# Kernel optimization log

Measured on AMD Instinct MI355X. Metric: run time of the kernel, lower is better.

## Reference

```python
import jax, jax.numpy as jnp
import numpy as np

N, F, FH, H = 4096, 512, 64, 8  # nodes, in-features, per-head out-features, heads
ALPHA = 0.2  # LeakyReLU slope


def setup_inputs() -> dict:
    key = jax.random.key(0)
    ks = jax.random.split(key, 6)
    X = jax.random.normal(ks[0], (N, F), dtype=jnp.float32)
    A = (jax.random.uniform(ks[1], (N, N)) < 0.02).astype(jnp.float32)
    glorot_w = (2.0 / (F + FH)) ** 0.5
    glorot_a = (2.0 / (FH + 1)) ** 0.5
    W = jax.random.normal(ks[2], (H, F, FH), dtype=jnp.float32) * glorot_w
    a_self = jax.random.normal(ks[3], (H, FH), dtype=jnp.float32) * glorot_a
    a_neigh = jax.random.normal(ks[4], (H, FH), dtype=jnp.float32) * glorot_a
    b = jnp.zeros((H, FH), dtype=jnp.float32)
    return {"X": X, "A": A, "W": W, "a_self": a_self, "a_neigh": a_neigh, "b": b}


def reference(X, A, W, a_self, a_neigh, b):
    # per-head linear projection: [H, N, FH]
    feats = jnp.einsum('nf,hfo->hno', X, W)
    s_self = jnp.einsum('hno,ho->hn', feats, a_self)    # [H, N]
    s_neigh = jnp.einsum('hno,ho->hn', feats, a_neigh)  # [H, N]
    # additive logits: self_i + neigh_j -> [H, N, N]
    dense = s_self[:, :, None] + s_neigh[:, None, :]
    dense = jnp.where(dense > 0, dense, ALPHA * dense)  # LeakyReLU(0.2)
    dense = dense * A[None, :, :]                       # multiplicative adjacency (as in source)
    attn = jax.nn.softmax(dense, axis=-1)               # full-row softmax (as in source)
    # dropout is identity at inference
    out = jnp.einsum('hij,hjo->hio', attn, feats) + b[:, None, :]  # [H, N, FH]
    out = jnp.transpose(out, (1, 0, 2)).reshape(N, H * FH)         # concat heads
    return jax.nn.relu(out)
```

## Files before the change

kernel.cpp:

```cpp
#include <hip/hip_runtime.h>
#include <hip/hip_bf16.h>

#define N_NODES 4096
#define F_IN 512
#define FHD 64
#define H_HEADS 8
#define C_OUT 512
#define ALPHA 0.2f
#define MAXE 192

typedef __attribute__((ext_vector_type(8))) short bf16x8;
typedef __attribute__((ext_vector_type(4))) float f32x4;

static __device__ __forceinline__ unsigned short f2bf(float f) {
  __hip_bfloat16 h = __float2bfloat16(f);
  union { __hip_bfloat16 h; unsigned short u; } cvt;
  cvt.h = h;
  return cvt.u;
}
static __device__ __forceinline__ float bf2f(unsigned short u) {
  return __uint_as_float(((unsigned)u) << 16);
}

__global__ __launch_bounds__(256) void conv_kernel(
    const float* __restrict__ X, const float* __restrict__ W,
    unsigned short* __restrict__ Xb, unsigned short* __restrict__ WbT,
    float* __restrict__ colsum) {
  __shared__ float sT[64][65];
  const int bid = blockIdx.x;
  const int tid = threadIdx.x;
  if (bid < 2048) {
    int idx = bid * 256 + tid;
    float4 v = reinterpret_cast<const float4*>(X)[idx];
    ushort4 u;
    u.x = f2bf(v.x); u.y = f2bf(v.y); u.z = f2bf(v.z); u.w = f2bf(v.w);
    reinterpret_cast<ushort4*>(Xb)[idx] = u;
  } else if (bid < 2048 + 64) {
    const int b2 = bid - 2048;
    const int fblk = b2 & 7, h = b2 >> 3;
#pragma unroll
    for (int i = 0; i < 16; ++i) {
      int idx = tid + i * 256;
      int f = idx >> 6, o = idx & 63;
      sT[f][o] = W[((size_t)h * F_IN + fblk * 64 + f) * FHD + o];
    }
    __syncthreads();
#pragma unroll
    for (int i = 0; i < 16; ++i) {
      int idx = tid + i * 256;
      int o = idx >> 6, f = idx & 63;
      WbT[(size_t)h * FHD * F_IN + (size_t)o * F_IN + fblk * 64 + f] =
          f2bf(sT[f][o]);
    }
  } else {
    colsum[tid] = 0.f;
    colsum[tid + 256] = 0.f;
  }
}

__global__ __launch_bounds__(256) void gemm_feats_mfma_kernel(
    const unsigned short* __restrict__ Xb, const unsigned short* __restrict__ WbT,
    const float* __restrict__ a_self, const float* __restrict__ a_neigh,
    unsigned short* __restrict__ featsb,
    float* __restrict__ s_self, float* __restrict__ s_neigh,
    float* __restrict__ colsum) {
  const int h = blockIdx.y;
  const int n0 = blockIdx.x * 64;
  __shared__ unsigned short sX[2][64 * 72];
  __shared__ unsigned short sW[2][64 * 72];
  __shared__ float sred[4][64];
  const int tid = threadIdx.x;
  const int wid = tid >> 6, lane = tid & 63;
  const int l15 = lane & 15, l4 = lane >> 4;

  const int row = tid >> 2, seg = (tid & 3) * 16;
  const unsigned short* xsrc = Xb + (size_t)(n0 + row) * F_IN + seg;
  const unsigned short* wsrc = WbT + ((size_t)h * FHD + row) * F_IN + seg;
  const int soff = row * 72 + seg;

  f32x4 acc[4];
#pragma unroll
  for (int j = 0; j < 4; ++j) acc[j] = (f32x4){0.f, 0.f, 0.f, 0.f};

  *(bf16x8*)&sX[0][soff] = *(const bf16x8*)(xsrc);
  *(bf16x8*)&sX[0][soff + 8] = *(const bf16x8*)(xsrc + 8);
  *(bf16x8*)&sW[0][soff] = *(const bf16x8*)(wsrc);
  *(bf16x8*)&sW[0][soff + 8] = *(const bf16x8*)(wsrc + 8);
  __syncthreads();

  int cur = 0;
  for (int s = 0; s < 8; ++s) {
    bf16x8 px0, px1, pw0, pw1;
    const bool pf = (s < 7);
    if (pf) {
      const int k = (s + 1) * 64;
      px0 = *(const bf16x8*)(xsrc + k);
      px1 = *(const bf16x8*)(xsrc + k + 8);
      pw0 = *(const bf16x8*)(wsrc + k);
      pw1 = *(const bf16x8*)(wsrc + k + 8);
    }
#pragma unroll
    for (int kk = 0; kk < 2; ++kk) {
      bf16x8 a = *(const bf16x8*)&sX[cur][(wid * 16 + l15) * 72 + kk * 32 + l4 * 8];
#pragma unroll
      for (int tn = 0; tn < 4; ++tn) {
        bf16x8 b = *(const bf16x8*)&sW[cur][(tn * 16 + l15) * 72 + kk * 32 + l4 * 8];
        acc[tn] =
            __builtin_amdgcn_mfma_f32_16x16x32_bf16(a, b, acc[tn], 0, 0, 0);
      }
    }
    if (pf) {
      *(bf16x8*)&sX[cur ^ 1][soff] = px0;
      *(bf16x8*)&sX[cur ^ 1][soff + 8] = px1;
      *(bf16x8*)&sW[cur ^ 1][soff] = pw0;
      *(bf16x8*)&sW[cur ^ 1][soff + 8] = pw1;
      __syncthreads();
      cur ^= 1;
    }
  }

  float aS[4], aN[4];
#pragma unroll
  for (int tn = 0; tn < 4; ++tn) {
    aS[tn] = a_self[h * FHD + tn * 16 + l15];
    aN[tn] = a_neigh[h * FHD + tn * 16 + l15];
  }
#pragma unroll
  for (int r = 0; r < 4; ++r) {
    const int grow = n0 + wid * 16 + l4 * 4 + r;
#pragma unroll
    for (int tn = 0; tn < 4; ++tn)
      featsb[(size_t)grow * C_OUT + h * FHD + tn * 16 + l15] =
          f2bf(acc[tn][r]);
    float ps = 0.f, pn = 0.f;
#pragma unroll
    for (int tn = 0; tn < 4; ++tn) {
      float v = acc[tn][r];
      ps = fmaf(v, aS[tn], ps);
      pn = fmaf(v, aN[tn], pn);
    }
#pragma unroll
    for (int sh = 1; sh < 16; sh <<= 1) {
      ps += __shfl_xor(ps, sh, 64);
      pn += __shfl_xor(pn, sh, 64);
    }
    if (l15 == 0) {
      s_self[grow * 8 + h] = ps;
      s_neigh[grow * 8 + h] = pn;
    }
  }

  float psum[4];
#pragma unroll
  for (int tn = 0; tn < 4; ++tn) {
    float s = acc[tn][0] + acc[tn][1] + acc[tn][2] + acc[tn][3];
    s += __shfl_xor(s, 16, 64);
    s += __shfl_xor(s, 32, 64);
    psum[tn] = s;
  }
  if (l4 == 0) {
#pragma unroll
    for (int tn = 0; tn < 4; ++tn) sred[wid][tn * 16 + l15] = psum[tn];
  }
  __syncthreads();
  if (tid < 64) {
    float s = sred[0][tid] + sred[1][tid] + sred[2][tid] + sred[3][tid];
    atomicAdd(&colsum[h * FHD + tid], s);
  }
}

__global__ __launch_bounds__(256) void attn_kernel(
    const float* __restrict__ A, const unsigned short* __restrict__ featsb,
    const float* __restrict__ s_self, const float* __restrict__ s_neigh,
    const float* __restrict__ colsum, const float* __restrict__ bias,
    float* __restrict__ out) {
  const int i = blockIdx.x;
  const int tid = threadIdx.x;
  const int wid = tid >> 6, lane = tid & 63;
  __shared__ int s_idx[MAXE];
  __shared__ float s_w[MAXE][9];
  __shared__ int wave_tot[4];
  __shared__ float sh_self[8];
  __shared__ float sh_e0[8], sh_invZ[8];

  if (tid < 8) sh_self[tid] = s_self[i * 8 + tid];

  const float4* __restrict__ Arow4 =
      reinterpret_cast<const float4*>(A + (size_t)i * N_NODES);
  float4 v[4];
#pragma unroll
  for (int q = 0; q < 4; ++q) v[q] = Arow4[tid * 4 + q];
  int mask16 = 0;
#pragma unroll
  for (int q = 0; q < 4; ++q) {
    mask16 |= (v[q].x != 0.f) ? (1 << (q * 4 + 0)) : 0;
    mask16 |= (v[q].y != 0.f) ? (1 << (q * 4 + 1)) : 0;
    mask16 |= (v[q].z != 0.f) ? (1 << (q * 4 + 2)) : 0;
    mask16 |= (v[q].w != 0.f) ? (1 << (q * 4 + 3)) : 0;
  }
  int cnt = __popc(mask16);
  int inc = cnt;
#pragma unroll
  for (int s = 1; s < 64; s <<= 1) {
    int t = __shfl_up(inc, s, 64);
    if (lane >= s) inc += t;
  }
  if (lane == 63) wave_tot[wid] = inc;
  __syncthreads();
  int wprefix = 0, tot = 0;
#pragma unroll
  for (int w = 0; w < 4; ++w) {
    int t = wave_tot[w];
    if (w < wid) wprefix += t;
    tot += t;
  }
  int pos = wprefix + inc - cnt;
  const int jbase = tid * 16;
  while (mask16) {
    int k = __ffs(mask16) - 1;
    mask16 &= mask16 - 1;
    if (pos < MAXE) s_idx[pos] = jbase + k;
    ++pos;
  }
  const int deg = tot < MAXE ? tot : MAXE;
  __syncthreads();

  for (int k = tid; k < deg * 8; k += 256) {
    int e = k >> 3, h = k & 7;
    int j = s_idx[e];
    float l = sh_self[h] + s_neigh[j * 8 + h];
    s_w[e][h] = l > 0.f ? l : ALPHA * l;
  }
  __syncthreads();

#pragma unroll
  for (int p = 0; p < 2; ++p) {
    const int h = wid * 2 + p;
    float m = -1e30f;
    for (int e = lane; e < deg; e += 64) m = fmaxf(m, s_w[e][h]);
#pragma unroll
    for (int s = 32; s > 0; s >>= 1) m = fmaxf(m, __shfl_xor(m, s, 64));
    m = fmaxf(m, 0.0f);
    float e0 = __expf(-m);
    float zs = 0.f;
    for (int e = lane; e < deg; e += 64) {
      float w = __expf(s_w[e][h] - m);
      s_w[e][h] = w - e0;
      zs += w;
    }
#pragma unroll
    for (int s = 32; s > 0; s >>= 1) zs += __shfl_xor(zs, s, 64);
    if (lane == 0) {
      sh_e0[h] = e0;
      sh_invZ[h] = 1.0f / (zs + (float)(N_NODES - deg) * e0);
    }
  }
  __syncthreads();

  const int h = tid >> 5;
  const float e0 = sh_e0[h], invZ = sh_invZ[h];
  const float2 cs = *reinterpret_cast<const float2*>(&colsum[tid * 2]);
  const ushort2* __restrict__ fb = reinterpret_cast<const ushort2*>(featsb);
  float ax0 = e0 * cs.x, ay0 = e0 * cs.y;
  float ax1 = 0.f, ay1 = 0.f, ax2 = 0.f, ay2 = 0.f, ax3 = 0.f, ay3 = 0.f;
  int e = 0;
  for (; e + 3 < deg; e += 4) {
    int j0 = s_idx[e], j1 = s_idx[e + 1], j2 = s_idx[e + 2], j3 = s_idx[e + 3];
    float w0 = s_w[e][h], w1 = s_w[e + 1][h];
    float w2 = s_w[e + 2][h], w3 = s_w[e + 3][h];
    ushort2 u0 = fb[(size_t)j0 * 256 + tid];
    ushort2 u1 = fb[(size_t)j1 * 256 + tid];
    ushort2 u2 = fb[(size_t)j2 * 256 + tid];
    ushort2 u3 = fb[(size_t)j3 * 256 + tid];
    ax0 = fmaf(w0, bf2f(u0.x), ax0);
    ay0 = fmaf(w0, bf2f(u0.y), ay0);
    ax1 = fmaf(w1, bf2f(u1.x), ax1);
    ay1 = fmaf(w1, bf2f(u1.y), ay1);
    ax2 = fmaf(w2, bf2f(u2.x), ax2);
    ay2 = fmaf(w2, bf2f(u2.y), ay2);
    ax3 = fmaf(w3, bf2f(u3.x), ax3);
    ay3 = fmaf(w3, bf2f(u3.y), ay3);
  }
  for (; e < deg; ++e) {
    float w0 = s_w[e][h];
    ushort2 u0 = fb[(size_t)s_idx[e] * 256 + tid];
    ax0 = fmaf(w0, bf2f(u0.x), ax0);
    ay0 = fmaf(w0, bf2f(u0.y), ay0);
  }
  const float2 bb = *reinterpret_cast<const float2*>(&bias[tid * 2]);
  float vx = ((ax0 + ax1) + (ax2 + ax3)) * invZ + bb.x;
  float vy = ((ay0 + ay1) + (ay2 + ay3)) * invZ + bb.y;
  float2 o;
  o.x = vx > 0.f ? vx : 0.f;
  o.y = vy > 0.f ? vy : 0.f;
  *reinterpret_cast<float2*>(&out[(size_t)i * C_OUT + tid * 2]) = o;
}

extern "C" void kernel_launch(void* const* d_in, const int* in_sizes, int n_in,
                              void* d_out, int out_size, void* d_ws, size_t ws_size,
                              hipStream_t stream) {
  const float* X = (const float*)d_in[0];
  const float* A = (const float*)d_in[1];
  const float* W = (const float*)d_in[2];
  const float* a_self = (const float*)d_in[3];
  const float* a_neigh = (const float*)d_in[4];
  const float* b = (const float*)d_in[5];
  float* out = (float*)d_out;

  char* ws = (char*)d_ws;
  unsigned short* featsb = (unsigned short*)ws;
  char* p = ws + (size_t)N_NODES * C_OUT * 2;
  float* s_self = (float*)p;  p += N_NODES * H_HEADS * 4;
  float* s_neigh = (float*)p; p += N_NODES * H_HEADS * 4;
  float* colsum = (float*)p;  p += C_OUT * 4;
  unsigned short* WbT = (unsigned short*)p;

  unsigned short* Xb = (unsigned short*)d_out;

  conv_kernel<<<2048 + 64 + 1, 256, 0, stream>>>(X, W, Xb, WbT, colsum);
  gemm_feats_mfma_kernel<<<dim3(64, 8), 256, 0, stream>>>(
      Xb, WbT, a_self, a_neigh, featsb, s_self, s_neigh, colsum);
  attn_kernel<<<N_NODES, 256, 0, stream>>>(A, featsb, s_self, s_neigh, colsum,
                                           b, out);
}
```

Before: 60.51 us.

## Move adjacency row scan into GEMM launch to overlap with projection

```diff
diff --git a/kernel.cpp b/kernel.cpp
--- a/kernel.cpp
+++ b/kernel.cpp
@@ -8,6 +8,7 @@
 #define C_OUT 512
 #define ALPHA 0.2f
 #define MAXE 192
+#define GEMM_BLOCKS 512
 
 typedef __attribute__((ext_vector_type(8))) short bf16x8;
 typedef __attribute__((ext_vector_type(4))) float f32x4;
@@ -58,19 +59,68 @@
   }
 }
 
-__global__ __launch_bounds__(256) void gemm_feats_mfma_kernel(
+__global__ __launch_bounds__(256) void gemm_scan_kernel(
     const unsigned short* __restrict__ Xb, const unsigned short* __restrict__ WbT,
     const float* __restrict__ a_self, const float* __restrict__ a_neigh,
+    const float* __restrict__ A,
     unsigned short* __restrict__ featsb,
     float* __restrict__ s_self, float* __restrict__ s_neigh,
-    float* __restrict__ colsum) {
-  const int h = blockIdx.y;
-  const int n0 = blockIdx.x * 64;
+    float* __restrict__ colsum,
+    unsigned short* __restrict__ edges, int* __restrict__ degs) {
   __shared__ unsigned short sX[2][64 * 72];
   __shared__ unsigned short sW[2][64 * 72];
   __shared__ float sred[4][64];
+  const int bid = blockIdx.x;
   const int tid = threadIdx.x;
   const int wid = tid >> 6, lane = tid & 63;
+
+  if (bid >= GEMM_BLOCKS) {
+    const int i = bid - GEMM_BLOCKS;
+    int* wave_tot = reinterpret_cast<int*>(&sred[0][0]);
+    const float4* __restrict__ Arow4 =
+        reinterpret_cast<const float4*>(A + (size_t)i * N_NODES);
+    float4 v[4];
+#pragma unroll
+    for (int q = 0; q < 4; ++q) v[q] = Arow4[tid * 4 + q];
+    int mask16 = 0;
+#pragma unroll
+    for (int q = 0; q < 4; ++q) {
+      mask16 |= (v[q].x != 0.f) ? (1 << (q * 4 + 0)) : 0;
+      mask16 |= (v[q].y != 0.f) ? (1 << (q * 4 + 1)) : 0;
+      mask16 |= (v[q].z != 0.f) ? (1 << (q * 4 + 2)) : 0;
+      mask16 |= (v[q].w != 0.f) ? (1 << (q * 4 + 3)) : 0;
+    }
+    int cnt = __popc(mask16);
+    int inc = cnt;
+#pragma unroll
+    for (int s = 1; s < 64; s <<= 1) {
+      int t = __shfl_up(inc, s, 64);
+      if (lane >= s) inc += t;
+    }
+    if (lane == 63) wave_tot[wid] = inc;
+    __syncthreads();
+    int wprefix = 0, tot = 0;
+#pragma unroll
+    for (int w = 0; w < 4; ++w) {
+      int t = wave_tot[w];
+      if (w < wid) wprefix += t;
+      tot += t;
+    }
+    int pos = wprefix + inc - cnt;
+    const int jbase = tid * 16;
+    unsigned short* __restrict__ erow = edges + (size_t)i * MAXE;
+    while (mask16) {
+      int k = __ffs(mask16) - 1;
+      mask16 &= mask16 - 1;
+      if (pos < MAXE) erow[pos] = (unsigned short)(jbase + k);
+      ++pos;
+    }
+    if (tid == 0) degs[i] = tot < MAXE ? tot : MAXE;
+    return;
+  }
+
+  const int h = bid >> 6;
+  const int n0 = (bid & 63) * 64;
   const int l15 = lane & 15, l4 = lane >> 4;
 
   const int row = tid >> 2, seg = (tid & 3) * 16;
@@ -158,6 +208,7 @@
     s += __shfl_xor(s, 32, 64);
     psum[tn] = s;
   }
+  __syncthreads();
   if (l4 == 0) {
 #pragma unroll
     for (int tn = 0; tn < 4; ++tn) sred[wid][tn * 16 + l15] = psum[tn];
@@ -170,7 +221,8 @@
 }
 
 __global__ __launch_bounds__(256) void attn_kernel(
-    const float* __restrict__ A, const unsigned short* __restrict__ featsb,
+    const unsigned short* __restrict__ edges, const int* __restrict__ degs,
+    const unsigned short* __restrict__ featsb,
     const float* __restrict__ s_self, const float* __restrict__ s_neigh,
     const float* __restrict__ colsum, const float* __restrict__ bias,
     float* __restrict__ out) {
@@ -179,50 +231,12 @@
   const int wid = tid >> 6, lane = tid & 63;
   __shared__ int s_idx[MAXE];
   __shared__ float s_w[MAXE][9];
-  __shared__ int wave_tot[4];
   __shared__ float sh_self[8];
   __shared__ float sh_e0[8], sh_invZ[8];
 
+  const int deg = degs[i];
   if (tid < 8) sh_self[tid] = s_self[i * 8 + tid];
-
-  const float4* __restrict__ Arow4 =
-      reinterpret_cast<const float4*>(A + (size_t)i * N_NODES);
-  float4 v[4];
-#pragma unroll
-  for (int q = 0; q < 4; ++q) v[q] = Arow4[tid * 4 + q];
-  int mask16 = 0;
-#pragma unroll
-  for (int q = 0; q < 4; ++q) {
-    mask16 |= (v[q].x != 0.f) ? (1 << (q * 4 + 0)) : 0;
-    mask16 |= (v[q].y != 0.f) ? (1 << (q * 4 + 1)) : 0;
-    mask16 |= (v[q].z != 0.f) ? (1 << (q * 4 + 2)) : 0;
-    mask16 |= (v[q].w != 0.f) ? (1 << (q * 4 + 3)) : 0;
-  }
-  int cnt = __popc(mask16);
-  int inc = cnt;
-#pragma unroll
-  for (int s = 1; s < 64; s <<= 1) {
-    int t = __shfl_up(inc, s, 64);
-    if (lane >= s) inc += t;
-  }
-  if (lane == 63) wave_tot[wid] = inc;
-  __syncthreads();
-  int wprefix = 0, tot = 0;
-#pragma unroll
-  for (int w = 0; w < 4; ++w) {
-    int t = wave_tot[w];
-    if (w < wid) wprefix += t;
-    tot += t;
-  }
-  int pos = wprefix + inc - cnt;
-  const int jbase = tid * 16;
-  while (mask16) {
-    int k = __ffs(mask16) - 1;
-    mask16 &= mask16 - 1;
-    if (pos < MAXE) s_idx[pos] = jbase + k;
-    ++pos;
-  }
-  const int deg = tot < MAXE ? tot : MAXE;
+  if (tid < deg) s_idx[tid] = edges[(size_t)i * MAXE + tid];
   __syncthreads();
 
   for (int k = tid; k < deg * 8; k += 256) {
@@ -313,13 +327,17 @@
   float* s_self = (float*)p;  p += N_NODES * H_HEADS * 4;
   float* s_neigh = (float*)p; p += N_NODES * H_HEADS * 4;
   float* colsum = (float*)p;  p += C_OUT * 4;
+  int* degs = (int*)p;        p += N_NODES * 4;
+  unsigned short* edges = (unsigned short*)p;
+  p += (size_t)N_NODES * MAXE * 2;
   unsigned short* WbT = (unsigned short*)p;
 
   unsigned short* Xb = (unsigned short*)d_out;
 
   conv_kernel<<<2048 + 64 + 1, 256, 0, stream>>>(X, W, Xb, WbT, colsum);
-  gemm_feats_mfma_kernel<<<dim3(64, 8), 256, 0, stream>>>(
-      Xb, WbT, a_self, a_neigh, featsb, s_self, s_neigh, colsum);
-  attn_kernel<<<N_NODES, 256, 0, stream>>>(A, featsb, s_self, s_neigh, colsum,
-                                           b, out);
-}
+  gemm_scan_kernel<<<GEMM_BLOCKS + N_NODES, 256, 0, stream>>>(
+      Xb, WbT, a_self, a_neigh, A, featsb, s_self, s_neigh, colsum, edges,
+      degs);
+  attn_kernel<<<N_NODES, 256, 0, stream>>>(edges, degs, featsb, s_self,
+                                           s_neigh, colsum, b, out);
+}
```

Measured after the change: 55.76 us. 7.9% less time.

## Move adjacency scan into first kernel and split attention gather across 512 threads

Applied to the files above, without the earlier changes.

```diff
diff --git a/kernel.cpp b/kernel.cpp
--- a/kernel.cpp
+++ b/kernel.cpp
@@ -22,21 +22,66 @@
   return __uint_as_float(((unsigned)u) << 16);
 }
 
-__global__ __launch_bounds__(256) void conv_kernel(
-    const float* __restrict__ X, const float* __restrict__ W,
-    unsigned short* __restrict__ Xb, unsigned short* __restrict__ WbT,
-    float* __restrict__ colsum) {
+__global__ __launch_bounds__(256) void stream_kernel(
+    const float* __restrict__ A, const float* __restrict__ X,
+    const float* __restrict__ W, unsigned short* __restrict__ edges,
+    int* __restrict__ degs, unsigned short* __restrict__ Xb,
+    unsigned short* __restrict__ WbT, float* __restrict__ colsum) {
+  __shared__ int wave_tot[4];
   __shared__ float sT[64][65];
   const int bid = blockIdx.x;
   const int tid = threadIdx.x;
-  if (bid < 2048) {
-    int idx = bid * 256 + tid;
+
+  if (bid < N_NODES) {
+    const int i = bid;
+    const int wid = tid >> 6, lane = tid & 63;
+    const float4* __restrict__ Arow4 =
+        reinterpret_cast<const float4*>(A + (size_t)i * N_NODES);
+    float4 v[4];
+#pragma unroll
+    for (int q = 0; q < 4; ++q) v[q] = Arow4[tid * 4 + q];
+    int mask16 = 0;
+#pragma unroll
+    for (int q = 0; q < 4; ++q) {
+      mask16 |= (v[q].x != 0.f) ? (1 << (q * 4 + 0)) : 0;
+      mask16 |= (v[q].y != 0.f) ? (1 << (q * 4 + 1)) : 0;
+      mask16 |= (v[q].z != 0.f) ? (1 << (q * 4 + 2)) : 0;
+      mask16 |= (v[q].w != 0.f) ? (1 << (q * 4 + 3)) : 0;
+    }
+    int cnt = __popc(mask16);
+    int inc = cnt;
+#pragma unroll
+    for (int s = 1; s < 64; s <<= 1) {
+      int t = __shfl_up(inc, s, 64);
+      if (lane >= s) inc += t;
+    }
+    if (lane == 63) wave_tot[wid] = inc;
+    __syncthreads();
+    int wprefix = 0, tot = 0;
+#pragma unroll
+    for (int w = 0; w < 4; ++w) {
+      int t = wave_tot[w];
+      if (w < wid) wprefix += t;
+      tot += t;
+    }
+    int pos = wprefix + inc - cnt;
+    const int jbase = tid * 16;
+    unsigned short* __restrict__ erow = edges + (size_t)i * MAXE;
+    while (mask16) {
+      int k = __ffs(mask16) - 1;
+      mask16 &= mask16 - 1;
+      if (pos < MAXE) erow[pos] = (unsigned short)(jbase + k);
+      ++pos;
+    }
+    if (tid == 0) degs[i] = tot < MAXE ? tot : MAXE;
+  } else if (bid < N_NODES + 2048) {
+    int idx = (bid - N_NODES) * 256 + tid;
     float4 v = reinterpret_cast<const float4*>(X)[idx];
     ushort4 u;
     u.x = f2bf(v.x); u.y = f2bf(v.y); u.z = f2bf(v.z); u.w = f2bf(v.w);
     reinterpret_cast<ushort4*>(Xb)[idx] = u;
-  } else if (bid < 2048 + 64) {
-    const int b2 = bid - 2048;
+  } else if (bid < N_NODES + 2048 + 64) {
+    const int b2 = bid - (N_NODES + 2048);
     const int fblk = b2 & 7, h = b2 >> 3;
 #pragma unroll
     for (int i = 0; i < 16; ++i) {
@@ -169,8 +214,9 @@
   }
 }
 
-__global__ __launch_bounds__(256) void attn_kernel(
-    const float* __restrict__ A, const unsigned short* __restrict__ featsb,
+__global__ __launch_bounds__(512) void attn_kernel(
+    const unsigned short* __restrict__ edges, const int* __restrict__ degs,
+    const unsigned short* __restrict__ featsb,
     const float* __restrict__ s_self, const float* __restrict__ s_neigh,
     const float* __restrict__ colsum, const float* __restrict__ bias,
     float* __restrict__ out) {
@@ -179,53 +225,16 @@
   const int wid = tid >> 6, lane = tid & 63;
   __shared__ int s_idx[MAXE];
   __shared__ float s_w[MAXE][9];
-  __shared__ int wave_tot[4];
   __shared__ float sh_self[8];
   __shared__ float sh_e0[8], sh_invZ[8];
-
+  __shared__ float s_part[256][2];
+
+  const int deg = degs[i];
   if (tid < 8) sh_self[tid] = s_self[i * 8 + tid];
-
-  const float4* __restrict__ Arow4 =
-      reinterpret_cast<const float4*>(A + (size_t)i * N_NODES);
-  float4 v[4];
-#pragma unroll
-  for (int q = 0; q < 4; ++q) v[q] = Arow4[tid * 4 + q];
-  int mask16 = 0;
-#pragma unroll
-  for (int q = 0; q < 4; ++q) {
-    mask16 |= (v[q].x != 0.f) ? (1 << (q * 4 + 0)) : 0;
-    mask16 |= (v[q].y != 0.f) ? (1 << (q * 4 + 1)) : 0;
-    mask16 |= (v[q].z != 0.f) ? (1 << (q * 4 + 2)) : 0;
-    mask16 |= (v[q].w != 0.f) ? (1 << (q * 4 + 3)) : 0;
-  }
-  int cnt = __popc(mask16);
-  int inc = cnt;
-#pragma unroll
-  for (int s = 1; s < 64; s <<= 1) {
-    int t = __shfl_up(inc, s, 64);
-    if (lane >= s) inc += t;
-  }
-  if (lane == 63) wave_tot[wid] = inc;
-  __syncthreads();
-  int wprefix = 0, tot = 0;
-#pragma unroll
-  for (int w = 0; w < 4; ++w) {
-    int t = wave_tot[w];
-    if (w < wid) wprefix += t;
-    tot += t;
-  }
-  int pos = wprefix + inc - cnt;
-  const int jbase = tid * 16;
-  while (mask16) {
-    int k = __ffs(mask16) - 1;
-    mask16 &= mask16 - 1;
-    if (pos < MAXE) s_idx[pos] = jbase + k;
-    ++pos;
-  }
-  const int deg = tot < MAXE ? tot : MAXE;
-  __syncthreads();
-
-  for (int k = tid; k < deg * 8; k += 256) {
+  if (tid < deg) s_idx[tid] = edges[(size_t)i * MAXE + tid];
+  __syncthreads();
+
+  for (int k = tid; k < deg * 8; k += 512) {
     int e = k >> 3, h = k & 7;
     int j = s_idx[e];
     float l = sh_self[h] + s_neigh[j * 8 + h];
@@ -233,9 +242,8 @@
   }
   __syncthreads();
 
-#pragma unroll
-  for (int p = 0; p < 2; ++p) {
-    const int h = wid * 2 + p;
+  {
+    const int h = wid;
     float m = -1e30f;
     for (int e = lane; e < deg; e += 64) m = fmaxf(m, s_w[e][h]);
 #pragma unroll
@@ -257,21 +265,24 @@
   }
   __syncthreads();
 
-  const int h = tid >> 5;
-  const float e0 = sh_e0[h], invZ = sh_invZ[h];
-  const float2 cs = *reinterpret_cast<const float2*>(&colsum[tid * 2]);
+  const int cp = tid & 255;
+  const int half = tid >> 8;
+  const int h = cp >> 5;
+  const int dhalf = (deg + 1) >> 1;
+  const int ebeg = half ? dhalf : 0;
+  const int eend = half ? deg : dhalf;
   const ushort2* __restrict__ fb = reinterpret_cast<const ushort2*>(featsb);
-  float ax0 = e0 * cs.x, ay0 = e0 * cs.y;
-  float ax1 = 0.f, ay1 = 0.f, ax2 = 0.f, ay2 = 0.f, ax3 = 0.f, ay3 = 0.f;
-  int e = 0;
-  for (; e + 3 < deg; e += 4) {
+  float ax0 = 0.f, ay0 = 0.f, ax1 = 0.f, ay1 = 0.f;
+  float ax2 = 0.f, ay2 = 0.f, ax3 = 0.f, ay3 = 0.f;
+  int e = ebeg;
+  for (; e + 3 < eend; e += 4) {
     int j0 = s_idx[e], j1 = s_idx[e + 1], j2 = s_idx[e + 2], j3 = s_idx[e + 3];
     float w0 = s_w[e][h], w1 = s_w[e + 1][h];
     float w2 = s_w[e + 2][h], w3 = s_w[e + 3][h];
-    ushort2 u0 = fb[(size_t)j0 * 256 + tid];
-    ushort2 u1 = fb[(size_t)j1 * 256 + tid];
-    ushort2 u2 = fb[(size_t)j2 * 256 + tid];
-    ushort2 u3 = fb[(size_t)j3 * 256 + tid];
+    ushort2 u0 = fb[(size_t)j0 * 256 + cp];
+    ushort2 u1 = fb[(size_t)j1 * 256 + cp];
+    ushort2 u2 = fb[(size_t)j2 * 256 + cp];
+    ushort2 u3 = fb[(size_t)j3 * 256 + cp];
     ax0 = fmaf(w0, bf2f(u0.x), ax0);
     ay0 = fmaf(w0, bf2f(u0.y), ay0);
     ax1 = fmaf(w1, bf2f(u1.x), ax1);
@@ -281,19 +292,32 @@
     ax3 = fmaf(w3, bf2f(u3.x), ax3);
     ay3 = fmaf(w3, bf2f(u3.y), ay3);
   }
-  for (; e < deg; ++e) {
+  for (; e < eend; ++e) {
     float w0 = s_w[e][h];
-    ushort2 u0 = fb[(size_t)s_idx[e] * 256 + tid];
+    ushort2 u0 = fb[(size_t)s_idx[e] * 256 + cp];
     ax0 = fmaf(w0, bf2f(u0.x), ax0);
     ay0 = fmaf(w0, bf2f(u0.y), ay0);
   }
-  const float2 bb = *reinterpret_cast<const float2*>(&bias[tid * 2]);
-  float vx = ((ax0 + ax1) + (ax2 + ax3)) * invZ + bb.x;
-  float vy = ((ay0 + ay1) + (ay2 + ay3)) * invZ + bb.y;
-  float2 o;
-  o.x = vx > 0.f ? vx : 0.f;
-  o.y = vy > 0.f ? vy : 0.f;
-  *reinterpret_cast<float2*>(&out[(size_t)i * C_OUT + tid * 2]) = o;
+  float ax = (ax0 + ax1) + (ax2 + ax3);
+  float ay = (ay0 + ay1) + (ay2 + ay3);
+  if (half) {
+    s_part[cp][0] = ax;
+    s_part[cp][1] = ay;
+  }
+  __syncthreads();
+  if (!half) {
+    const float e0 = sh_e0[h], invZ = sh_invZ[h];
+    const float2 cs = *reinterpret_cast<const float2*>(&colsum[cp * 2]);
+    ax += s_part[cp][0] + e0 * cs.x;
+    ay += s_part[cp][1] + e0 * cs.y;
+    const float2 bb = *reinterpret_cast<const float2*>(&bias[cp * 2]);
+    float vx = ax * invZ + bb.x;
+    float vy = ay * invZ + bb.y;
+    float2 o;
+    o.x = vx > 0.f ? vx : 0.f;
+    o.y = vy > 0.f ? vy : 0.f;
+    *reinterpret_cast<float2*>(&out[(size_t)i * C_OUT + cp * 2]) = o;
+  }
 }
 
 extern "C" void kernel_launch(void* const* d_in, const int* in_sizes, int n_in,
@@ -313,13 +337,17 @@
   float* s_self = (float*)p;  p += N_NODES * H_HEADS * 4;
   float* s_neigh = (float*)p; p += N_NODES * H_HEADS * 4;
   float* colsum = (float*)p;  p += C_OUT * 4;
+  int* degs = (int*)p;        p += N_NODES * 4;
+  unsigned short* edges = (unsigned short*)p;
+  p += (size_t)N_NODES * MAXE * 2;
   unsigned short* WbT = (unsigned short*)p;
 
   unsigned short* Xb = (unsigned short*)d_out;
 
-  conv_kernel<<<2048 + 64 + 1, 256, 0, stream>>>(X, W, Xb, WbT, colsum);
+  stream_kernel<<<N_NODES + 2048 + 64 + 1, 256, 0, stream>>>(
+      A, X, W, edges, degs, Xb, WbT, colsum);
   gemm_feats_mfma_kernel<<<dim3(64, 8), 256, 0, stream>>>(
       Xb, WbT, a_self, a_neigh, featsb, s_self, s_neigh, colsum);
-  attn_kernel<<<N_NODES, 256, 0, stream>>>(A, featsb, s_self, s_neigh, colsum,
-                                           b, out);
-}
+  attn_kernel<<<N_NODES, 512, 0, stream>>>(edges, degs, featsb, s_self,
+                                           s_neigh, colsum, b, out);
+}
```

New measurement: 64.38 us. +6.4%, slower.
